# Performance work log

Measured on AMD Instinct MI355X. Metric: run time of the kernel, lower is better.

The kernel has to match this reference:

```python
import jax, jax.numpy as jnp
import numpy as np

D = 1024        # hidden_size = input_size = output_size
E = 8           # num_experts
K = 2           # top-k
TEMP = 1.0      # router temperature


def setup_inputs() -> dict:
    key = jax.random.key(0)
    ks = jax.random.split(key, 7)
    s = 0.02
    x = jax.random.normal(ks[0], (4, 2048, D), dtype=jnp.float32)
    w_router = jax.random.normal(ks[1], (D, E), dtype=jnp.float32) * s
    w1 = jax.random.normal(ks[2], (E, D, D), dtype=jnp.float32) * s
    b1 = jnp.zeros((E, D), dtype=jnp.float32)
    w2 = jax.random.normal(ks[3], (E, D, D), dtype=jnp.float32) * s
    b2 = jnp.zeros((E, D), dtype=jnp.float32)
    return {"x": x, "w_router": w_router, "w1": w1, "b1": b1, "w2": w2, "b2": b2}


def reference(x, w_router, w1, b1, w2, b2):
    B, S, _ = x.shape
    # Router: temperature-scaled logits, softmax, top-k
    logits = jnp.einsum('bsd,de->bse', x, w_router) / TEMP          # [B,S,E]
    probs = jax.nn.softmax(logits, axis=-1)
    top_k_probs, top_k_idx = jax.lax.top_k(probs, K)                # [B,S,K]
    xt = x.reshape(-1, D)                                           # [T,D]
    idx = top_k_idx.reshape(-1, K)                                  # [T,K]
    pk = top_k_probs.reshape(-1, K)                                 # [T,K]
    # Dense expert eval: every expert on every token (faithful to source)
    h = jax.nn.gelu(jnp.einsum('td,edh->eth', xt, w1) + b1[:, None, :])
    expert_out = jnp.einsum('eth,ehd->etd', h, w2) + b2[:, None, :]  # [E,T,D]
    expert_out = jnp.transpose(expert_out, (1, 0, 2))                # [T,E,D]
    # Gather selected experts and combine with routing probs
    sel = jnp.take_along_axis(expert_out, idx[:, :, None], axis=1)   # [T,K,D]
    combined = jnp.sum(sel * pk[:, :, None], axis=1)                 # [T,D]
    return combined.reshape(B, S, D), logits
```

## Files before the change

### kernel.cpp

```cpp
#include <hip/hip_runtime.h>
#include <hip/hip_bf16.h>

#define DH 1024
#define NE 8
#define NT 8192
#define NTK 16384
#define BM 128
#define BN 256
#define NSUB 32

typedef __bf16 bf16x8 __attribute__((ext_vector_type(8)));
typedef float f32x4 __attribute__((ext_vector_type(4)));
typedef unsigned short u16;
typedef u16 u16x8 __attribute__((ext_vector_type(8)));
typedef u16 u16x4 __attribute__((ext_vector_type(4)));

__device__ __forceinline__ u16 f2bf(float f) {
  union { float f; unsigned u; } v; v.f = f;
  return (u16)((v.u + 0x7fffu + ((v.u >> 16) & 1u)) >> 16);
}
__device__ __forceinline__ float bf2f(u16 h) {
  union { unsigned u; float f; } v; v.u = ((unsigned)h) << 16;
  return v.f;
}
__device__ __forceinline__ float gelu_tanh(float v) {
  float y = 0.7978845608028654f * (v + 0.044715f * v * v * v);
  float t = 1.f - 2.f / (1.f + __expf(2.f * y));
  return 0.5f * v * (1.f + t);
}

__device__ __forceinline__ void gload_lds16(const u16* g, u16* l) {
  __builtin_amdgcn_global_load_lds(
      (const __attribute__((address_space(1))) void*)g,
      (__attribute__((address_space(3))) void*)l, 16, 0, 0);
}

__global__ __launch_bounds__(256) void prep_transpose(
    const float* __restrict__ w1, const float* __restrict__ w2,
    u16* __restrict__ w1t, u16* __restrict__ w2t) {
  __shared__ float tile[64][65];
  int z = blockIdx.z;
  const float* src = (z < NE) ? (w1 + (size_t)z * DH * DH) : (w2 + (size_t)(z - NE) * DH * DH);
  u16* dst = (z < NE) ? (w1t + (size_t)z * DH * DH) : (w2t + (size_t)(z - NE) * DH * DH);
  int d0 = blockIdx.y * 64, n0 = blockIdx.x * 64;
  int tid = threadIdx.x;
  int r16 = tid >> 4;
  int c4 = (tid & 15) * 4;
#pragma unroll
  for (int it = 0; it < 4; ++it) {
    int rr = it * 16 + r16;
    float4 v = *(const float4*)&src[(size_t)(d0 + rr) * DH + n0 + c4];
    tile[rr][c4] = v.x; tile[rr][c4 + 1] = v.y;
    tile[rr][c4 + 2] = v.z; tile[rr][c4 + 3] = v.w;
  }
  __syncthreads();
#pragma unroll
  for (int it = 0; it < 4; ++it) {
    int n = it * 16 + r16;
    u16x4 o;
    o[0] = f2bf(tile[c4][n]);     o[1] = f2bf(tile[c4 + 1][n]);
    o[2] = f2bf(tile[c4 + 2][n]); o[3] = f2bf(tile[c4 + 3][n]);
    *(u16x4*)&dst[(size_t)(n0 + n) * DH + d0 + c4] = o;
  }
}

__global__ __launch_bounds__(256) void router_kernel(
    const float* __restrict__ x, const float* __restrict__ wr,
    float* __restrict__ logits_out, int* __restrict__ tkidx,
    float* __restrict__ tkp, int* __restrict__ counts,
    u16* __restrict__ xb) {
  __shared__ float wsh[NE][DH + 8];
  __shared__ int hist[NE];
  int tid = threadIdx.x;
  for (int i = tid; i < DH * NE; i += 256) {
    int d = i >> 3, e = i & 7;
    wsh[e][d] = wr[i];
  }
  if (tid < NE) hist[tid] = 0;
  __syncthreads();

  int lane = tid & 63;
  int wv = tid >> 6;
  int t0 = blockIdx.x * 32 + wv * 8;
#pragma unroll 1
  for (int i = 0; i < 8; ++i) {
    int t = t0 + i;
    const float4* xp = (const float4*)(x + (size_t)t * DH);
    u16* xbrow = xb + (size_t)t * DH;
    float a[8] = {0.f, 0.f, 0.f, 0.f, 0.f, 0.f, 0.f, 0.f};
#pragma unroll
    for (int it = 0; it < 4; ++it) {
      float4 xv = xp[it * 64 + lane];
      int d0 = (it * 64 + lane) * 4;
      u16x4 c4;
      c4[0] = f2bf(xv.x); c4[1] = f2bf(xv.y); c4[2] = f2bf(xv.z); c4[3] = f2bf(xv.w);
      *(u16x4*)(xbrow + d0) = c4;
#pragma unroll
      for (int e = 0; e < 8; ++e) {
        float4 w4 = *(const float4*)&wsh[e][d0];
        a[e] += xv.x * w4.x + xv.y * w4.y + xv.z * w4.z + xv.w * w4.w;
      }
    }
#pragma unroll
    for (int off = 32; off; off >>= 1) {
#pragma unroll
      for (int e = 0; e < 8; ++e) a[e] += __shfl_xor(a[e], off, 64);
    }
    if (lane < 8) logits_out[(size_t)t * NE + lane] = a[lane];
    if (lane == 0) {
      float m1 = a[0]; int i1 = 0;
#pragma unroll
      for (int e = 1; e < 8; ++e) if (a[e] > m1) { m1 = a[e]; i1 = e; }
      float m2 = -3.4e38f; int i2 = 0;
#pragma unroll
      for (int e = 0; e < 8; ++e) if (e != i1 && a[e] > m2) { m2 = a[e]; i2 = e; }
      float den = 0.f;
#pragma unroll
      for (int e = 0; e < 8; ++e) den += expf(a[e] - m1);
      tkidx[2 * t] = i1; tkidx[2 * t + 1] = i2;
      tkp[2 * t] = 1.0f / den;
      tkp[2 * t + 1] = expf(m2 - m1) / den;
      atomicAdd(&hist[i1], 1);
      atomicAdd(&hist[i2], 1);
    }
  }
  __syncthreads();
  if (tid < NE) atomicAdd(&counts[tid], hist[tid]);
}

__global__ void offsets_kernel(const int* __restrict__ counts,
                               int* __restrict__ offs, int* __restrict__ cur,
                               int* __restrict__ tmap) {
  if (threadIdx.x == 0) {
    int s = 0;
    for (int e = 0; e < NE; ++e) { offs[e] = s; s += counts[e]; cur[e] = 0; }
    offs[NE] = s;
    int t = 0;
    for (int e = 0; e < NE; ++e)
      for (int m0 = 0; m0 < counts[e]; m0 += BM) {
        tmap[1 + 2 * t] = e; tmap[2 + 2 * t] = m0; ++t;
      }
    tmap[0] = t;
  }
}

__global__ __launch_bounds__(1024) void scatter_kernel(
    const int* __restrict__ tkidx, const float* __restrict__ tkp,
    const int* __restrict__ offs, int* __restrict__ cur,
    int* __restrict__ rows, int* __restrict__ posof, float* __restrict__ pp) {
  __shared__ int h[NE];
  __shared__ int base[NE];
  int tid = threadIdx.x;
  int gid = blockIdx.x * 1024 + tid;
  if (tid < NE) h[tid] = 0;
  __syncthreads();
  int e = tkidx[gid];
  int myrank = atomicAdd(&h[e], 1);
  __syncthreads();
  if (tid < NE) base[tid] = atomicAdd(&cur[tid], h[tid]);
  __syncthreads();
  int pos = offs[e] + base[e] + myrank;
  rows[pos] = gid >> 1;
  posof[gid] = pos;
  pp[pos] = tkp[gid];
}

template <int GELU>
__global__ __launch_bounds__(512, 4) void gemm_kernel(
    const u16* __restrict__ A, const u16* __restrict__ W,
    const float* __restrict__ bias, const int* __restrict__ counts,
    const int* __restrict__ offs, const int* __restrict__ rows,
    const int* __restrict__ tmap, u16* __restrict__ outb) {
  int orig = blockIdx.y * 4 + blockIdx.x;
  int wg = (orig & 7) * 68 + (orig >> 3);
  int tx = wg & 3, ty = wg >> 2;
  if (ty >= tmap[0]) return;
  int e = tmap[1 + 2 * ty];
  int m0 = tmap[2 + 2 * ty];
  int cnt = counts[e];
  int seg = offs[e];
  int n0 = tx * BN;

  __shared__ __attribute__((aligned(16))) u16 lds[3][12288];

  int tid = threadIdx.x;
  int lane = tid & 63;
  int wv = tid >> 6;

  int srow = tid >> 2;
  int sc8 = ((tid & 3) ^ ((srow >> 1) & 3)) * 8;
  int gi = m0 + srow;
  int cl = gi < cnt ? gi : cnt - 1;
  int arow = GELU ? rows[seg + cl] : (seg + cl);
  const u16* aSrc = A + (size_t)arow * DH + sc8;
  const u16* bSrc0 = W + (size_t)e * DH * DH + (size_t)(n0 + srow) * DH + sc8;
  const u16* bSrc1 = bSrc0 + (size_t)128 * DH;

  int wb = wv * 512;
  auto stage = [&](int slot, int s) {
    int k0 = s * 32;
    u16* base = &lds[slot][0];
    gload_lds16(aSrc + k0, base + wb);
    gload_lds16(bSrc0 + k0, base + 4096 + wb);
    gload_lds16(bSrc1 + k0, base + 8192 + wb);
  };

  int lr = lane & 15;
  int quad = lane >> 4;
  int chunkOff = (quad ^ ((lr >> 1) & 3)) * 8;
  int wm = wv >> 2, wn = wv & 3;
  int wrr = wm * 64, wcc = wn * 64;

  int aOff[4], bOff[4];
#pragma unroll
  for (int m = 0; m < 4; ++m) aOff[m] = (wrr + m * 16 + lr) * 32 + chunkOff;
#pragma unroll
  for (int n = 0; n < 4; ++n) bOff[n] = 4096 + (wcc + n * 16 + lr) * 32 + chunkOff;

  f32x4 acc[4][4] = {};

  stage(0, 0);
  stage(1, 1);

#pragma unroll 1
  for (int s = 0; s < NSUB; ++s) {
    if (s + 2 < NSUB) stage((s + 2) % 3, s + 2);
    asm volatile("s_waitcnt vmcnt(6)" ::: "memory");
    __builtin_amdgcn_s_barrier();
    const u16* S = &lds[s % 3][0];
    bf16x8 af[4], bf[4];
#pragma unroll
    for (int m = 0; m < 4; ++m) af[m] = *(const bf16x8*)(S + aOff[m]);
#pragma unroll
    for (int n = 0; n < 4; ++n) bf[n] = *(const bf16x8*)(S + bOff[n]);
    __builtin_amdgcn_s_setprio(1);
#pragma unroll
    for (int m = 0; m < 4; ++m)
#pragma unroll
      for (int n = 0; n < 4; ++n)
        acc[m][n] = __builtin_amdgcn_mfma_f32_16x16x32_bf16(af[m], bf[n], acc[m][n], 0, 0, 0);
    __builtin_amdgcn_s_setprio(0);
    __builtin_amdgcn_s_barrier();
  }

  int r4 = quad * 4;
  const float* be = bias + (size_t)e * DH;
#pragma unroll
  for (int m = 0; m < 4; ++m) {
#pragma unroll
    for (int n = 0; n < 4; ++n) {
      int col = n0 + wcc + n * 16 + lr;
      float bvv = be[col];
#pragma unroll
      for (int j = 0; j < 4; ++j) {
        int gr = m0 + wrr + m * 16 + r4 + j;
        if (gr < cnt) {
          float v = acc[m][n][j] + bvv;
          if (GELU) v = gelu_tanh(v);
          outb[(size_t)(seg + gr) * DH + col] = f2bf(v);
        }
      }
    }
  }
}

__global__ __launch_bounds__(256) void combine_kernel(
    const u16* __restrict__ eo, const float* __restrict__ tkp,
    const int* __restrict__ posof, float* __restrict__ out) {
  int gid = blockIdx.x * 256 + threadIdx.x;
  int t = gid >> 8;
  int n = (gid & 255) * 4;
  float p0 = tkp[2 * t], p1 = tkp[2 * t + 1];
  int q0 = posof[2 * t], q1 = posof[2 * t + 1];
  u16x4 a = *(const u16x4*)(eo + (size_t)q0 * DH + n);
  u16x4 b = *(const u16x4*)(eo + (size_t)q1 * DH + n);
  float4 o;
  o.x = p0 * bf2f(a[0]) + p1 * bf2f(b[0]);
  o.y = p0 * bf2f(a[1]) + p1 * bf2f(b[1]);
  o.z = p0 * bf2f(a[2]) + p1 * bf2f(b[2]);
  o.w = p0 * bf2f(a[3]) + p1 * bf2f(b[3]);
  *(float4*)(out + (size_t)t * DH + n) = o;
}

extern "C" void kernel_launch(void* const* d_in, const int* in_sizes, int n_in,
                              void* d_out, int out_size, void* d_ws, size_t ws_size,
                              hipStream_t stream) {
  const float* x = (const float*)d_in[0];
  const float* w_router = (const float*)d_in[1];
  const float* w1 = (const float*)d_in[2];
  const float* b1 = (const float*)d_in[3];
  const float* w2 = (const float*)d_in[4];
  const float* b2 = (const float*)d_in[5];
  float* out = (float*)d_out;
  float* logits = out + (size_t)NT * DH;

  char* ws = (char*)d_ws;
  size_t off = 0;
  auto alloc = [&](size_t bytes) -> void* {
    void* p = ws + off;
    off = (off + bytes + 255) & ~(size_t)255;
    return p;
  };
  int* ctrl = (int*)alloc(256);
  int* counts = ctrl;
  int* cur = ctrl + 8;
  int* offs = ctrl + 16;
  int* tmap = (int*)alloc(2048);
  int* tkidx = (int*)alloc((size_t)NTK * 4);
  float* tkp = (float*)alloc((size_t)NTK * 4);
  int* rows = (int*)alloc((size_t)NTK * 4);
  int* posof = (int*)alloc((size_t)NTK * 4);
  float* pp = (float*)alloc((size_t)NTK * 4);
  u16* w1t = (u16*)alloc((size_t)NE * DH * DH * 2);
  u16* w2t = (u16*)alloc((size_t)NE * DH * DH * 2);
  u16* hbuf = (u16*)alloc((size_t)NTK * DH * 2);
  u16* eo = (u16*)alloc((size_t)NTK * DH * 2);
  u16* xb = eo;

  hipMemsetAsync(ctrl, 0, 256, stream);

  prep_transpose<<<dim3(16, 16, 16), 256, 0, stream>>>(w1, w2, w1t, w2t);
  router_kernel<<<NT / 32, 256, 0, stream>>>(x, w_router, logits, tkidx, tkp, counts, xb);
  offsets_kernel<<<1, 64, 0, stream>>>(counts, offs, cur, tmap);
  scatter_kernel<<<NTK / 1024, 1024, 0, stream>>>(tkidx, tkp, offs, cur, rows, posof, pp);
  gemm_kernel<1><<<dim3(4, 136, 1), 512, 0, stream>>>(xb, w1t, b1, counts, offs, rows, tmap, hbuf);
  gemm_kernel<0><<<dim3(4, 136, 1), 512, 0, stream>>>(hbuf, w2t, b2, counts, offs, rows, tmap, eo);
  combine_kernel<<<NT, 256, 0, stream>>>(eo, tkp, posof, out);
}
```

Before: 196.2 us.

## Halve GEMM workgroup to 4 waves with larger per-wave 128x64 tiles

The expert GEMM kernel now runs 256 threads (4 waves) instead of 512 per 128x256 tile. Each wave computes a 128x64 output slice, holding an 8x4 accumulator array, so each B fragment is reused across twice as many MFMAs. Each thread issues six async global-to-LDS loads per stage instead of three, and the last two k-steps are peeled out of the loop with matching vmcnt waits. This raises register pressure per wave and lowers occupancy (launch bounds 256,2) in exchange for fewer LDS reads per MFMA and fewer waves to synchronise.

Measured after the change: 209.8 us. 1.07x slower.

```diff
diff --git a/kernel.cpp b/kernel.cpp
--- a/kernel.cpp
+++ b/kernel.cpp
@@ -166,7 +166,7 @@
 }
 
 template <int GELU>
-__global__ __launch_bounds__(512, 4) void gemm_kernel(
+__global__ __launch_bounds__(256, 2) void gemm_kernel(
     const u16* __restrict__ A, const u16* __restrict__ W,
     const float* __restrict__ bias, const int* __restrict__ counts,
     const int* __restrict__ offs, const int* __restrict__ rows,
@@ -188,72 +188,89 @@
   int wv = tid >> 6;
 
   int srow = tid >> 2;
-  int sc8 = ((tid & 3) ^ ((srow >> 1) & 3)) * 8;
-  int gi = m0 + srow;
-  int cl = gi < cnt ? gi : cnt - 1;
-  int arow = GELU ? rows[seg + cl] : (seg + cl);
-  const u16* aSrc = A + (size_t)arow * DH + sc8;
-  const u16* bSrc0 = W + (size_t)e * DH * DH + (size_t)(n0 + srow) * DH + sc8;
-  const u16* bSrc1 = bSrc0 + (size_t)128 * DH;
+  int sc8 = ((tid & 3) ^ ((tid >> 3) & 3)) * 8;
+  int gi0 = m0 + srow, gi1 = m0 + 64 + srow;
+  int cl0 = gi0 < cnt ? gi0 : cnt - 1;
+  int cl1 = gi1 < cnt ? gi1 : cnt - 1;
+  int arow0 = GELU ? rows[seg + cl0] : (seg + cl0);
+  int arow1 = GELU ? rows[seg + cl1] : (seg + cl1);
+  const u16* aSrc0 = A + (size_t)arow0 * DH + sc8;
+  const u16* aSrc1 = A + (size_t)arow1 * DH + sc8;
+  const u16* wBase = W + (size_t)e * DH * DH + (size_t)(n0 + srow) * DH + sc8;
+  const u16* bSrc0 = wBase;
+  const u16* bSrc1 = wBase + (size_t)64 * DH;
+  const u16* bSrc2 = wBase + (size_t)128 * DH;
+  const u16* bSrc3 = wBase + (size_t)192 * DH;
 
   int wb = wv * 512;
   auto stage = [&](int slot, int s) {
     int k0 = s * 32;
     u16* base = &lds[slot][0];
-    gload_lds16(aSrc + k0, base + wb);
+    gload_lds16(aSrc0 + k0, base + wb);
+    gload_lds16(aSrc1 + k0, base + 2048 + wb);
     gload_lds16(bSrc0 + k0, base + 4096 + wb);
-    gload_lds16(bSrc1 + k0, base + 8192 + wb);
+    gload_lds16(bSrc1 + k0, base + 6144 + wb);
+    gload_lds16(bSrc2 + k0, base + 8192 + wb);
+    gload_lds16(bSrc3 + k0, base + 10240 + wb);
   };
 
   int lr = lane & 15;
   int quad = lane >> 4;
   int chunkOff = (quad ^ ((lr >> 1) & 3)) * 8;
-  int wm = wv >> 2, wn = wv & 3;
-  int wrr = wm * 64, wcc = wn * 64;
-
-  int aOff[4], bOff[4];
-#pragma unroll
-  for (int m = 0; m < 4; ++m) aOff[m] = (wrr + m * 16 + lr) * 32 + chunkOff;
+  int wcc = wv * 64;
+
+  int aOff[8], bOff[4];
+#pragma unroll
+  for (int m = 0; m < 8; ++m) aOff[m] = (m * 16 + lr) * 32 + chunkOff;
 #pragma unroll
   for (int n = 0; n < 4; ++n) bOff[n] = 4096 + (wcc + n * 16 + lr) * 32 + chunkOff;
 
-  f32x4 acc[4][4] = {};
-
-  stage(0, 0);
-  stage(1, 1);
-
-#pragma unroll 1
-  for (int s = 0; s < NSUB; ++s) {
-    if (s + 2 < NSUB) stage((s + 2) % 3, s + 2);
-    asm volatile("s_waitcnt vmcnt(6)" ::: "memory");
-    __builtin_amdgcn_s_barrier();
-    const u16* S = &lds[s % 3][0];
-    bf16x8 af[4], bf[4];
-#pragma unroll
-    for (int m = 0; m < 4; ++m) af[m] = *(const bf16x8*)(S + aOff[m]);
+  f32x4 acc[8][4] = {};
+
+  auto computeSub = [&](const u16* S) {
+    bf16x8 af[8], bf[4];
 #pragma unroll
     for (int n = 0; n < 4; ++n) bf[n] = *(const bf16x8*)(S + bOff[n]);
+#pragma unroll
+    for (int m = 0; m < 8; ++m) af[m] = *(const bf16x8*)(S + aOff[m]);
     __builtin_amdgcn_s_setprio(1);
 #pragma unroll
-    for (int m = 0; m < 4; ++m)
+    for (int m = 0; m < 8; ++m)
 #pragma unroll
       for (int n = 0; n < 4; ++n)
         acc[m][n] = __builtin_amdgcn_mfma_f32_16x16x32_bf16(af[m], bf[n], acc[m][n], 0, 0, 0);
     __builtin_amdgcn_s_setprio(0);
+  };
+
+  stage(0, 0);
+  stage(1, 1);
+#pragma unroll 1
+  for (int s = 0; s < NSUB - 2; ++s) {
+    stage((s + 2) % 3, s + 2);
+    asm volatile("s_waitcnt vmcnt(12)" ::: "memory");
     __builtin_amdgcn_s_barrier();
-  }
+    computeSub(&lds[s % 3][0]);
+    __builtin_amdgcn_s_barrier();
+  }
+  asm volatile("s_waitcnt vmcnt(6)" ::: "memory");
+  __builtin_amdgcn_s_barrier();
+  computeSub(&lds[(NSUB - 2) % 3][0]);
+  __builtin_amdgcn_s_barrier();
+  asm volatile("s_waitcnt vmcnt(0)" ::: "memory");
+  __builtin_amdgcn_s_barrier();
+  computeSub(&lds[(NSUB - 1) % 3][0]);
 
   int r4 = quad * 4;
   const float* be = bias + (size_t)e * DH;
 #pragma unroll
-  for (int m = 0; m < 4; ++m) {
+  for (int m = 0; m < 8; ++m) {
 #pragma unroll
     for (int n = 0; n < 4; ++n) {
       int col = n0 + wcc + n * 16 + lr;
       float bvv = be[col];
 #pragma unroll
       for (int j = 0; j < 4; ++j) {
-        int gr = m0 + wrr + m * 16 + r4 + j;
+        int gr = m0 + m * 16 + r4 + j;
         if (gr < cnt) {
           float v = acc[m][n][j] + bvv;
           if (GELU) v = gelu_tanh(v);
@@ -323,7 +340,7 @@
   router_kernel<<<NT / 32, 256, 0, stream>>>(x, w_router, logits, tkidx, tkp, counts, xb);
   offsets_kernel<<<1, 64, 0, stream>>>(counts, offs, cur, tmap);
   scatter_kernel<<<NTK / 1024, 1024, 0, stream>>>(tkidx, tkp, offs, cur, rows, posof, pp);
-  gemm_kernel<1><<<dim3(4, 136, 1), 512, 0, stream>>>(xb, w1t, b1, counts, offs, rows, tmap, hbuf);
-  gemm_kernel<0><<<dim3(4, 136, 1), 512, 0, stream>>>(hbuf, w2t, b2, counts, offs, rows, tmap, eo);
+  gemm_kernel<1><<<dim3(4, 136, 1), 256, 0, stream>>>(xb, w1t, b1, counts, offs, rows, tmap, hbuf);
+  gemm_kernel<0><<<dim3(4, 136, 1), 256, 0, stream>>>(hbuf, w2t, b2, counts, offs, rows, tmap, eo);
   combine_kernel<<<NT, 256, 0, stream>>>(eo, tkp, posof, out);
 }
```

## Index GEMM tiles directly by expert grid and peel pipeline tail

Applied to the files above, without the earlier changes.

Drops the serial tile-map construction in the offsets kernel. The grouped GEMMs now launch an 8x544 grid indexed by expert and tile, and blocks beyond each expert's tile count exit immediately. The k-loop tail is also peeled so the last two sub-steps skip the conditional stage and wait with tighter vmcnt values. This removes a single-thread serial loop and a dependent tmap lookup, but launches many empty blocks and gives up the XCD-aware block swizzle, which may hurt L2 locality of the weights.

After: 182.0 us. -7.3%, faster.

```diff
diff --git a/kernel.cpp b/kernel.cpp
--- a/kernel.cpp
+++ b/kernel.cpp
@@ -129,18 +129,11 @@
 }
 
 __global__ void offsets_kernel(const int* __restrict__ counts,
-                               int* __restrict__ offs, int* __restrict__ cur,
-                               int* __restrict__ tmap) {
+                               int* __restrict__ offs, int* __restrict__ cur) {
   if (threadIdx.x == 0) {
     int s = 0;
     for (int e = 0; e < NE; ++e) { offs[e] = s; s += counts[e]; cur[e] = 0; }
     offs[NE] = s;
-    int t = 0;
-    for (int e = 0; e < NE; ++e)
-      for (int m0 = 0; m0 < counts[e]; m0 += BM) {
-        tmap[1 + 2 * t] = e; tmap[2 + 2 * t] = m0; ++t;
-      }
-    tmap[0] = t;
   }
 }
 
@@ -170,16 +163,15 @@
     const u16* __restrict__ A, const u16* __restrict__ W,
     const float* __restrict__ bias, const int* __restrict__ counts,
     const int* __restrict__ offs, const int* __restrict__ rows,
-    const int* __restrict__ tmap, u16* __restrict__ outb) {
-  int orig = blockIdx.y * 4 + blockIdx.x;
-  int wg = (orig & 7) * 68 + (orig >> 3);
-  int tx = wg & 3, ty = wg >> 2;
-  if (ty >= tmap[0]) return;
-  int e = tmap[1 + 2 * ty];
-  int m0 = tmap[2 + 2 * ty];
+    u16* __restrict__ outb) {
+  int e = blockIdx.x;
+  int q = blockIdx.y;
   int cnt = counts[e];
+  int nm = (cnt + BM - 1) / BM;
+  if (q >= nm * 4) return;
+  int m0 = (q >> 2) * BM;
+  int n0 = (q & 3) * BN;
   int seg = offs[e];
-  int n0 = tx * BN;
 
   __shared__ __attribute__((aligned(16))) u16 lds[3][12288];
 
@@ -219,15 +211,7 @@
 
   f32x4 acc[4][4] = {};
 
-  stage(0, 0);
-  stage(1, 1);
-
-#pragma unroll 1
-  for (int s = 0; s < NSUB; ++s) {
-    if (s + 2 < NSUB) stage((s + 2) % 3, s + 2);
-    asm volatile("s_waitcnt vmcnt(6)" ::: "memory");
-    __builtin_amdgcn_s_barrier();
-    const u16* S = &lds[s % 3][0];
+  auto computeSub = [&](const u16* S) {
     bf16x8 af[4], bf[4];
 #pragma unroll
     for (int m = 0; m < 4; ++m) af[m] = *(const bf16x8*)(S + aOff[m]);
@@ -240,8 +224,25 @@
       for (int n = 0; n < 4; ++n)
         acc[m][n] = __builtin_amdgcn_mfma_f32_16x16x32_bf16(af[m], bf[n], acc[m][n], 0, 0, 0);
     __builtin_amdgcn_s_setprio(0);
+  };
+
+  stage(0, 0);
+  stage(1, 1);
+#pragma unroll 1
+  for (int s = 0; s < NSUB - 2; ++s) {
+    stage((s + 2) % 3, s + 2);
+    asm volatile("s_waitcnt vmcnt(6)" ::: "memory");
     __builtin_amdgcn_s_barrier();
-  }
+    computeSub(&lds[s % 3][0]);
+    __builtin_amdgcn_s_barrier();
+  }
+  asm volatile("s_waitcnt vmcnt(3)" ::: "memory");
+  __builtin_amdgcn_s_barrier();
+  computeSub(&lds[(NSUB - 2) % 3][0]);
+  __builtin_amdgcn_s_barrier();
+  asm volatile("s_waitcnt vmcnt(0)" ::: "memory");
+  __builtin_amdgcn_s_barrier();
+  computeSub(&lds[(NSUB - 1) % 3][0]);
 
   int r4 = quad * 4;
   const float* be = bias + (size_t)e * DH;
@@ -305,7 +306,6 @@
   int* counts = ctrl;
   int* cur = ctrl + 8;
   int* offs = ctrl + 16;
-  int* tmap = (int*)alloc(2048);
   int* tkidx = (int*)alloc((size_t)NTK * 4);
   float* tkp = (float*)alloc((size_t)NTK * 4);
   int* rows = (int*)alloc((size_t)NTK * 4);
@@ -321,9 +321,9 @@
 
   prep_transpose<<<dim3(16, 16, 16), 256, 0, stream>>>(w1, w2, w1t, w2t);
   router_kernel<<<NT / 32, 256, 0, stream>>>(x, w_router, logits, tkidx, tkp, counts, xb);
-  offsets_kernel<<<1, 64, 0, stream>>>(counts, offs, cur, tmap);
+  offsets_kernel<<<1, 64, 0, stream>>>(counts, offs, cur);
   scatter_kernel<<<NTK / 1024, 1024, 0, stream>>>(tkidx, tkp, offs, cur, rows, posof, pp);
-  gemm_kernel<1><<<dim3(4, 136, 1), 512, 0, stream>>>(xb, w1t, b1, counts, offs, rows, tmap, hbuf);
-  gemm_kernel<0><<<dim3(4, 136, 1), 512, 0, stream>>>(hbuf, w2t, b2, counts, offs, rows, tmap, eo);
+  gemm_kernel<1><<<dim3(8, 544, 1), 512, 0, stream>>>(xb, w1t, b1, counts, offs, rows, hbuf);
+  gemm_kernel<0><<<dim3(8, 544, 1), 512, 0, stream>>>(hbuf, w2t, b2, counts, offs, rows, eo);
   combine_kernel<<<NT, 256, 0, stream>>>(eo, tkp, posof, out);
 }
```
